# Kernel tuning notes

Hardware: AMD Instinct MI355X
Metric: run time of the kernel (lower is better)

## Reference

```python
import jax, jax.numpy as jnp
import numpy as np

H, D_MODEL, LEN_Q, LEN_K, D_K, D_V = 16, 1024, 2048, 2048, 64, 64
BATCH = 4
SCALE = 1.0 / np.sqrt(float(D_K))


def setup_inputs() -> dict:
    key = jax.random.key(0)
    ks = jax.random.split(key, 10)
    inp = {
        "Q": jax.random.normal(ks[0], (BATCH, LEN_Q, D_MODEL), dtype=jnp.float32),
        "K": jax.random.normal(ks[1], (BATCH, LEN_K, D_MODEL), dtype=jnp.float32),
        "V": jax.random.normal(ks[2], (BATCH, LEN_K, D_MODEL), dtype=jnp.float32),
        "mask": jax.random.randint(ks[3], (BATCH, LEN_K), 0, 2, dtype=jnp.int32),
        # Linear params (torch Linear: y = x @ W.T + b); store W as [in, out].
        "Wq": jax.random.normal(ks[4], (D_MODEL, H * D_K), dtype=jnp.float32) * (1.0 / np.sqrt(D_MODEL)),
        "bq": jnp.zeros((H * D_K,), dtype=jnp.float32),
        "Wk": jax.random.normal(ks[5], (D_MODEL, H * D_K), dtype=jnp.float32) * (1.0 / np.sqrt(D_MODEL)),
        "bk": jnp.zeros((H * D_K,), dtype=jnp.float32),
        "Wv": jax.random.normal(ks[6], (D_MODEL, H * D_V), dtype=jnp.float32) * (1.0 / np.sqrt(D_MODEL)),
        "bv": jnp.zeros((H * D_V,), dtype=jnp.float32),
    }
    return inp


def reference(Q, K, V, mask, Wq, bq, Wk, bk, Wv, bv):
    B = Q.shape[0]
    # Projections -> [B, S, H, d]
    q = (Q @ Wq + bq).reshape(B, LEN_Q, H, D_K)
    k = (K @ Wk + bk).reshape(B, LEN_K, H, D_K)
    v = (V @ Wv + bv).reshape(B, LEN_K, H, D_V)
    # Scores: [B, H, len_q, len_k]
    scores = jnp.einsum("bqhd,bkhd->bhqk", q, k) * SCALE
    # Key-padding mask broadcast over heads and queries
    scores = jnp.where(mask[:, None, None, :] == 0, jnp.float32(-1e9), scores)
    alpha = jax.nn.softmax(scores, axis=-1)
    out = jnp.einsum("bhqk,bkhd->bqhd", alpha, v)  # [B, len_q, H, d_v]
    return out.reshape(B, LEN_Q, H * D_V)
```

## Files before the change

kernel.cpp:

```cpp
#include <hip/hip_runtime.h>

#define NH 16
#define DM 1024
#define SQ 2048
#define BT 4

typedef __attribute__((ext_vector_type(8))) short bf16x8;
typedef __attribute__((ext_vector_type(4))) short sh4;
typedef __attribute__((ext_vector_type(4))) float f4;
typedef __attribute__((ext_vector_type(4))) float fv4;
typedef __attribute__((ext_vector_type(4))) unsigned uv4;
typedef unsigned short u16;

#define M2BIAS 23.083120654f
#define SCALE2 0.18033688f

__device__ __forceinline__ u16 f2bf(float f) {
    union { float f; unsigned u; } v; v.f = f;
    unsigned r = v.u + 0x7FFFu + ((v.u >> 16) & 1u);
    return (u16)(r >> 16);
}

__device__ __forceinline__ float fast_exp2(float x) {
#if __has_builtin(__builtin_amdgcn_exp2f)
    return __builtin_amdgcn_exp2f(x);
#else
    return exp2f(x);
#endif
}

__device__ __forceinline__ int prem(int s) {
    return (s & ~31) | ((s & 4) << 2) | ((s >> 1) & 12) | (s & 3);
}

#define GLD16(gp, lp) __builtin_amdgcn_global_load_lds( \
    (const __attribute__((address_space(1))) void*)(gp), \
    (__attribute__((address_space(3))) void*)(lp), 16, 0, 0)

__global__ __launch_bounds__(256) void cvt_x(const float* __restrict__ x, u16* __restrict__ y) {
    int i = blockIdx.x * 256 + threadIdx.x;
    fv4 v = ((const fv4*)x)[i];
    sh4 r;
    r[0] = (short)f2bf(v[0]); r[1] = (short)f2bf(v[1]);
    r[2] = (short)f2bf(v[2]); r[3] = (short)f2bf(v[3]);
    ((sh4*)y)[i] = r;
}

__global__ __launch_bounds__(256) void cvt_wT(const float* __restrict__ Wsrc, u16* __restrict__ Wt) {
    __shared__ float t[64][65];
    int r0 = blockIdx.x * 64, c0 = blockIdx.y * 64;
    #pragma unroll
    for (int i = 0; i < 16; ++i) {
        int idx = i * 256 + threadIdx.x;
        int r = idx >> 6, c = idx & 63;
        t[r][c] = Wsrc[(size_t)(r0 + r) * DM + c0 + c];
    }
    __syncthreads();
    #pragma unroll
    for (int i = 0; i < 16; ++i) {
        int idx = i * 256 + threadIdx.x;
        int n = idx >> 6, k = idx & 63;
        Wt[(size_t)(c0 + n) * DM + r0 + k] = f2bf(t[k][n]);
    }
}

__global__ __launch_bounds__(256) void mk_mbias(const int* __restrict__ mask, float* __restrict__ mb) {
    int i = blockIdx.x * 256 + threadIdx.x;
    mb[prem(i)] = mask[i] ? -M2BIAS : -__builtin_inff();
}

__global__ __launch_bounds__(256) void gemm_proj(const u16* __restrict__ A, const u16* __restrict__ Bt,
                                                 const float* __restrict__ bias, u16* __restrict__ outp,
                                                 int vmode) {
    __shared__ u16 As[128 * 64];
    __shared__ u16 Bs[128 * 64];
    int tid = threadIdx.x;
    int w = tid >> 6, lane = tid & 63, quad = lane >> 4, l16 = lane & 15;
    int wm = w >> 1, wn = w & 1;
    int r8 = lane >> 3, cg = (lane & 7) ^ r8;
    const u16* Ag = A + (size_t)blockIdx.x * 128 * DM;
    const u16* Bg = Bt + (size_t)blockIdx.y * 128 * DM;

    f4 acc[4][4];
    #pragma unroll
    for (int mt = 0; mt < 4; ++mt)
        #pragma unroll
        for (int nt = 0; nt < 4; ++nt) acc[mt][nt] = f4{0.f, 0.f, 0.f, 0.f};

    for (int kt = 0; kt < 16; ++kt) {
        int kofs = kt * 64 + cg * 8;
        #pragma unroll
        for (int c = 0; c < 4; ++c) {
            int rbase = w * 32 + c * 8;
            GLD16(Ag + (size_t)(rbase + r8) * DM + kofs, &As[rbase * 64]);
            GLD16(Bg + (size_t)(rbase + r8) * DM + kofs, &Bs[rbase * 64]);
        }
        __syncthreads();
        #pragma unroll
        for (int ks = 0; ks < 2; ++ks) {
            bf16x8 afr[4], bfr[4];
            #pragma unroll
            for (int mt = 0; mt < 4; ++mt) {
                int row = wm * 64 + mt * 16 + l16;
                int ch = (ks * 4 + quad) ^ (row & 7);
                afr[mt] = *(const bf16x8*)&As[row * 64 + ch * 8];
            }
            #pragma unroll
            for (int nt = 0; nt < 4; ++nt) {
                int row = wn * 64 + nt * 16 + l16;
                int ch = (ks * 4 + quad) ^ (row & 7);
                bfr[nt] = *(const bf16x8*)&Bs[row * 64 + ch * 8];
            }
            #pragma unroll
            for (int mt = 0; mt < 4; ++mt)
                #pragma unroll
                for (int nt = 0; nt < 4; ++nt)
                    acc[mt][nt] = __builtin_amdgcn_mfma_f32_16x16x32_bf16(afr[mt], bfr[nt], acc[mt][nt], 0, 0, 0);
        }
        __syncthreads();
    }

    #pragma unroll
    for (int nt = 0; nt < 4; ++nt) {
        int ncol = blockIdx.y * 128 + wn * 64 + nt * 16 + l16;
        float bn = bias[ncol];
        int h = ncol >> 6, d = ncol & 63;
        #pragma unroll
        for (int mt = 0; mt < 4; ++mt) {
            int mbase = blockIdx.x * 128 + wm * 64 + mt * 16 + quad * 4;
            int bidx = mbase >> 11, s0 = mbase & 2047;
            if (vmode == 1) {
                sh4 pk;
                #pragma unroll
                for (int reg = 0; reg < 4; ++reg) pk[reg] = (short)f2bf(acc[mt][nt][reg] + bn);
                *(sh4*)&outp[(((size_t)bidx * NH + h) * 64 + d) * SQ + s0] = pk;
            } else {
                int sp = (vmode == 2) ? prem(s0) : s0;
                size_t base = ((size_t)bidx * NH + h) * SQ;
                #pragma unroll
                for (int reg = 0; reg < 4; ++reg)
                    outp[(base + sp + reg) * 64 + d] = f2bf(acc[mt][nt][reg] + bn);
            }
        }
    }
}

__global__ __launch_bounds__(256, 4) void attn(const u16* __restrict__ qw, const u16* __restrict__ kw,
                                               const u16* __restrict__ vtw, const float* __restrict__ mbias,
                                               float* __restrict__ outp) {
    __shared__ u16 Ks[2][64 * 64];
    __shared__ u16 Vs[2][64 * 64];
    int tid = threadIdx.x;
    int w = tid >> 6, lane = tid & 63, quad = lane >> 4, l16 = lane & 15;
    int r8 = lane >> 3, sl = lane & 7;
    int bh = blockIdx.x, b = bh >> 4;
    int h = bh & 15;
    int qbase = blockIdx.y * 128 + w * 32;
    const u16* qp = qw + (size_t)bh * SQ * 64;
    const u16* kp = kw + (size_t)bh * SQ * 64;
    const u16* vp = vtw + (size_t)bh * 64 * SQ;
    const float* mbp = mbias + b * SQ;

    bf16x8 aq[2][2];
    #pragma unroll
    for (int mt = 0; mt < 2; ++mt)
        #pragma unroll
        for (int ks = 0; ks < 2; ++ks)
            aq[mt][ks] = *(const bf16x8*)&qp[(size_t)(qbase + mt * 16 + l16) * 64 + ks * 32 + quad * 8];

    f4 o[2][4];
    float lrow[2] = {0.f, 0.f};
    #pragma unroll
    for (int mt = 0; mt < 2; ++mt)
        #pragma unroll
        for (int nt = 0; nt < 4; ++nt) o[mt][nt] = f4{0.f, 0.f, 0.f, 0.f};

    auto stage = [&](int buf, int k0) {
        #pragma unroll
        for (int j = 0; j < 2; ++j) {
            int row = w * 16 + j * 8 + r8;
            int gsl = sl ^ (row & 7);
            GLD16(kp + (size_t)(k0 + row) * 64 + gsl * 8, &Ks[buf][(w * 16 + j * 8) * 64]);
            GLD16(vp + (size_t)row * SQ + k0 + gsl * 8, &Vs[buf][(w * 16 + j * 8) * 64]);
        }
    };

    stage(0, 0);
    for (int kb = 0; kb < 32; ++kb) {
        int buf = kb & 1;
        int k0 = kb * 64;
        __syncthreads();
        fv4 bias4[4];
        #pragma unroll
        for (int kt = 0; kt < 4; ++kt)
            bias4[kt] = *(const fv4*)&mbp[k0 + kt * 16 + quad * 4];
        if (kb + 1 < 32) stage(buf ^ 1, k0 + 64);

        bf16x8 bk[4][2];
        #pragma unroll
        for (int kt = 0; kt < 4; ++kt)
            #pragma unroll
            for (int ks = 0; ks < 2; ++ks) {
                int r = kt * 16 + l16;
                int slot = (ks * 4 + quad) ^ (r & 7);
                bk[kt][ks] = *(const bf16x8*)&Ks[buf][r * 64 + slot * 8];
            }
        f4 S[4][2];
        #pragma unroll
        for (int kt = 0; kt < 4; ++kt)
            #pragma unroll
            for (int mt = 0; mt < 2; ++mt) {
                f4 s = f4{0.f, 0.f, 0.f, 0.f};
                s = __builtin_amdgcn_mfma_f32_16x16x32_bf16(bk[kt][0], aq[mt][0], s, 0, 0, 0);
                s = __builtin_amdgcn_mfma_f32_16x16x32_bf16(bk[kt][1], aq[mt][1], s, 0, 0, 0);
                S[kt][mt] = s;
            }
        bf16x8 pa8[2][2];
        #pragma unroll
        for (int g = 0; g < 2; ++g)
            #pragma unroll
            for (int mt = 0; mt < 2; ++mt) {
                f4 se = S[2 * g][mt], so = S[2 * g + 1][mt];
                float p0 = fast_exp2(se[0] * SCALE2 + bias4[2 * g][0]);
                float p1 = fast_exp2(se[1] * SCALE2 + bias4[2 * g][1]);
                float p2 = fast_exp2(se[2] * SCALE2 + bias4[2 * g][2]);
                float p3 = fast_exp2(se[3] * SCALE2 + bias4[2 * g][3]);
                float q0 = fast_exp2(so[0] * SCALE2 + bias4[2 * g + 1][0]);
                float q1 = fast_exp2(so[1] * SCALE2 + bias4[2 * g + 1][1]);
                float q2 = fast_exp2(so[2] * SCALE2 + bias4[2 * g + 1][2]);
                float q3 = fast_exp2(so[3] * SCALE2 + bias4[2 * g + 1][3]);
                lrow[mt] += ((p0 + p1) + (p2 + p3)) + ((q0 + q1) + (q2 + q3));
                uv4 wv;
                wv[0] = (__float_as_uint(p1) & 0xFFFF0000u) | (__float_as_uint(p0) >> 16);
                wv[1] = (__float_as_uint(p3) & 0xFFFF0000u) | (__float_as_uint(p2) >> 16);
                wv[2] = (__float_as_uint(q1) & 0xFFFF0000u) | (__float_as_uint(q0) >> 16);
                wv[3] = (__float_as_uint(q3) & 0xFFFF0000u) | (__float_as_uint(q2) >> 16);
                pa8[g][mt] = __builtin_bit_cast(bf16x8, wv);
            }
        #pragma unroll
        for (int g = 0; g < 2; ++g) {
            bf16x8 bv8[4];
            #pragma unroll
            for (int nt = 0; nt < 4; ++nt) {
                int row = nt * 16 + l16;
                int ch = (g * 4 + quad) ^ (row & 7);
                bv8[nt] = *(const bf16x8*)&Vs[buf][row * 64 + ch * 8];
            }
            #pragma unroll
            for (int mt = 0; mt < 2; ++mt)
                #pragma unroll
                for (int nt = 0; nt < 4; ++nt)
                    o[mt][nt] = __builtin_amdgcn_mfma_f32_16x16x32_bf16(pa8[g][mt], bv8[nt], o[mt][nt], 0, 0, 0);
        }
    }

    #pragma unroll
    for (int mt = 0; mt < 2; ++mt) {
        float v = lrow[mt];
        v += __shfl_xor(v, 16);
        v += __shfl_xor(v, 32);
        #pragma unroll
        for (int reg = 0; reg < 4; ++reg) {
            float inv = 1.f / __shfl(v, quad * 4 + reg);
            int row = qbase + mt * 16 + quad * 4 + reg;
            size_t obase = ((size_t)b * SQ + row) * DM + h * 64;
            #pragma unroll
            for (int nt = 0; nt < 4; ++nt)
                outp[obase + nt * 16 + l16] = o[mt][nt][reg] * inv;
        }
    }
}

extern "C" void kernel_launch(void* const* d_in, const int* in_sizes, int n_in,
                              void* d_out, int out_size, void* d_ws, size_t ws_size,
                              hipStream_t stream) {
    (void)in_sizes; (void)n_in; (void)out_size; (void)ws_size;
    const float* Q  = (const float*)d_in[0];
    const float* K  = (const float*)d_in[1];
    const float* V  = (const float*)d_in[2];
    const int* mask = (const int*)d_in[3];
    const float* Wq = (const float*)d_in[4];
    const float* bq = (const float*)d_in[5];
    const float* Wk = (const float*)d_in[6];
    const float* bk = (const float*)d_in[7];
    const float* Wv = (const float*)d_in[8];
    const float* bv = (const float*)d_in[9];
    float* out = (float*)d_out;
    char* ws = (char*)d_ws;
    u16* q_ws = (u16*)(ws);
    u16* k_ws = (u16*)(ws + (size_t)16 * 1024 * 1024);
    u16* v_ws = (u16*)(ws + (size_t)32 * 1024 * 1024);
    u16* xbuf = (u16*)(ws + (size_t)48 * 1024 * 1024);
    u16* wbuf = (u16*)(ws + (size_t)64 * 1024 * 1024);
    float* mb = (float*)(ws + (size_t)48 * 1024 * 1024);

    dim3 gGemm(64, 8), gW(16, 16);
    cvt_x<<<8192, 256, 0, stream>>>(Q, xbuf);
    cvt_wT<<<gW, 256, 0, stream>>>(Wq, wbuf);
    gemm_proj<<<gGemm, 256, 0, stream>>>(xbuf, wbuf, bq, q_ws, 0);
    cvt_x<<<8192, 256, 0, stream>>>(K, xbuf);
    cvt_wT<<<gW, 256, 0, stream>>>(Wk, wbuf);
    gemm_proj<<<gGemm, 256, 0, stream>>>(xbuf, wbuf, bk, k_ws, 2);
    cvt_x<<<8192, 256, 0, stream>>>(V, xbuf);
    cvt_wT<<<gW, 256, 0, stream>>>(Wv, wbuf);
    gemm_proj<<<gGemm, 256, 0, stream>>>(xbuf, wbuf, bv, v_ws, 1);
    mk_mbias<<<32, 256, 0, stream>>>(mask, mb);
    attn<<<dim3(64, 16), 256, 0, stream>>>(q_ws, k_ws, v_ws, mb, out);
}
```

Baseline: 339.1 us.

## Fuse fp32-to-bf16 activation conversion into a batched QKV projection GEMM

Drops the separate cvt_x passes. The projection GEMM now loads fp32 activations into registers, converts them with v_cvt_pk_bf16_f32, and writes them to LDS, prefetching the next k-tile in registers. The three weight transposes and three GEMMs are each batched into a single launch via blockIdx.z. This removes the bf16 intermediate round-trip through memory and cuts launch count, at the cost of more register pressure and a synchronous register-staged A path instead of direct global-to-LDS loads.

```diff
diff --git a/kernel.cpp b/kernel.cpp
--- a/kernel.cpp
+++ b/kernel.cpp
@@ -37,17 +37,11 @@
     (const __attribute__((address_space(1))) void*)(gp), \
     (__attribute__((address_space(3))) void*)(lp), 16, 0, 0)
 
-__global__ __launch_bounds__(256) void cvt_x(const float* __restrict__ x, u16* __restrict__ y) {
-    int i = blockIdx.x * 256 + threadIdx.x;
-    fv4 v = ((const fv4*)x)[i];
-    sh4 r;
-    r[0] = (short)f2bf(v[0]); r[1] = (short)f2bf(v[1]);
-    r[2] = (short)f2bf(v[2]); r[3] = (short)f2bf(v[3]);
-    ((sh4*)y)[i] = r;
-}
-
-__global__ __launch_bounds__(256) void cvt_wT(const float* __restrict__ Wsrc, u16* __restrict__ Wt) {
+__global__ __launch_bounds__(256) void cvt_wT3(const float* __restrict__ W0, const float* __restrict__ W1,
+                                               const float* __restrict__ W2, u16* __restrict__ Wt) {
     __shared__ float t[64][65];
+    const float* Wsrc = blockIdx.z == 0 ? W0 : (blockIdx.z == 1 ? W1 : W2);
+    u16* dst = Wt + (size_t)blockIdx.z * DM * DM;
     int r0 = blockIdx.x * 64, c0 = blockIdx.y * 64;
     #pragma unroll
     for (int i = 0; i < 16; ++i) {
@@ -60,7 +54,7 @@
     for (int i = 0; i < 16; ++i) {
         int idx = i * 256 + threadIdx.x;
         int n = idx >> 6, k = idx & 63;
-        Wt[(size_t)(c0 + n) * DM + r0 + k] = f2bf(t[k][n]);
+        dst[(size_t)(c0 + n) * DM + r0 + k] = f2bf(t[k][n]);
     }
 }
 
@@ -69,31 +63,59 @@
     mb[prem(i)] = mask[i] ? -M2BIAS : -__builtin_inff();
 }
 
-__global__ __launch_bounds__(256) void gemm_proj(const u16* __restrict__ A, const u16* __restrict__ Bt,
-                                                 const float* __restrict__ bias, u16* __restrict__ outp,
-                                                 int vmode) {
+__global__ __launch_bounds__(256, 3) void gemm3(const float* __restrict__ Qf, const float* __restrict__ Kf,
+                                                const float* __restrict__ Vf, const u16* __restrict__ Wt3,
+                                                const float* __restrict__ bq, const float* __restrict__ bk,
+                                                const float* __restrict__ bv, u16* __restrict__ out3) {
     __shared__ u16 As[128 * 64];
     __shared__ u16 Bs[128 * 64];
+    int z = blockIdx.z;
+    const float* Af = z == 0 ? Qf : (z == 1 ? Kf : Vf);
+    const float* bias = z == 0 ? bq : (z == 1 ? bk : bv);
+    int vmode = z == 0 ? 0 : (z == 1 ? 2 : 1);
+    const u16* Bg = Wt3 + (size_t)z * DM * DM + (size_t)blockIdx.y * 128 * DM;
+    u16* outp = out3 + (size_t)z * 8388608u;
+
     int tid = threadIdx.x;
     int w = tid >> 6, lane = tid & 63, quad = lane >> 4, l16 = lane & 15;
     int wm = w >> 1, wn = w & 1;
     int r8 = lane >> 3, cg = (lane & 7) ^ r8;
-    const u16* Ag = A + (size_t)blockIdx.x * 128 * DM;
-    const u16* Bg = Bt + (size_t)blockIdx.y * 128 * DM;
+
+    int arow0 = w * 32 + (lane >> 4);
+    int acol = (lane & 15) * 4;
+    const float* Ag = Af + (size_t)(blockIdx.x * 128 + arow0) * DM + acol;
+    int ach = (lane & 15) >> 1, asub = lane & 1;
 
     f4 acc[4][4];
     #pragma unroll
     for (int mt = 0; mt < 4; ++mt)
         #pragma unroll
         for (int nt = 0; nt < 4; ++nt) acc[mt][nt] = f4{0.f, 0.f, 0.f, 0.f};
+
+    fv4 ar[8];
+    #pragma unroll
+    for (int j = 0; j < 8; ++j) ar[j] = *(const fv4*)(Ag + (size_t)j * 4 * DM);
 
     for (int kt = 0; kt < 16; ++kt) {
         int kofs = kt * 64 + cg * 8;
         #pragma unroll
         for (int c = 0; c < 4; ++c) {
             int rbase = w * 32 + c * 8;
-            GLD16(Ag + (size_t)(rbase + r8) * DM + kofs, &As[rbase * 64]);
             GLD16(Bg + (size_t)(rbase + r8) * DM + kofs, &Bs[rbase * 64]);
+        }
+        #pragma unroll
+        for (int j = 0; j < 8; ++j) {
+            unsigned lo, hi;
+            asm("v_cvt_pk_bf16_f32 %0, %1, %2" : "=v"(lo) : "v"(ar[j][0]), "v"(ar[j][1]));
+            asm("v_cvt_pk_bf16_f32 %0, %1, %2" : "=v"(hi) : "v"(ar[j][2]), "v"(ar[j][3]));
+            int row = arow0 + j * 4;
+            uint2 pk; pk.x = lo; pk.y = hi;
+            *(uint2*)&As[row * 64 + (ach ^ (row & 7)) * 8 + asub * 4] = pk;
+        }
+        if (kt + 1 < 16) {
+            const float* src = Ag + (kt + 1) * 64;
+            #pragma unroll
+            for (int j = 0; j < 8; ++j) ar[j] = *(const fv4*)(src + (size_t)j * 4 * DM);
         }
         __syncthreads();
         #pragma unroll
@@ -287,23 +309,14 @@
     const float* bv = (const float*)d_in[9];
     float* out = (float*)d_out;
     char* ws = (char*)d_ws;
-    u16* q_ws = (u16*)(ws);
-    u16* k_ws = (u16*)(ws + (size_t)16 * 1024 * 1024);
-    u16* v_ws = (u16*)(ws + (size_t)32 * 1024 * 1024);
-    u16* xbuf = (u16*)(ws + (size_t)48 * 1024 * 1024);
-    u16* wbuf = (u16*)(ws + (size_t)64 * 1024 * 1024);
-    float* mb = (float*)(ws + (size_t)48 * 1024 * 1024);
-
-    dim3 gGemm(64, 8), gW(16, 16);
-    cvt_x<<<8192, 256, 0, stream>>>(Q, xbuf);
-    cvt_wT<<<gW, 256, 0, stream>>>(Wq, wbuf);
-    gemm_proj<<<gGemm, 256, 0, stream>>>(xbuf, wbuf, bq, q_ws, 0);
-    cvt_x<<<8192, 256, 0, stream>>>(K, xbuf);
-    cvt_wT<<<gW, 256, 0, stream>>>(Wk, wbuf);
-    gemm_proj<<<gGemm, 256, 0, stream>>>(xbuf, wbuf, bk, k_ws, 2);
-    cvt_x<<<8192, 256, 0, stream>>>(V, xbuf);
-    cvt_wT<<<gW, 256, 0, stream>>>(Wv, wbuf);
-    gemm_proj<<<gGemm, 256, 0, stream>>>(xbuf, wbuf, bv, v_ws, 1);
+    u16* q_ws  = (u16*)(ws);
+    u16* k_ws  = (u16*)(ws + (size_t)16 * 1024 * 1024);
+    u16* v_ws  = (u16*)(ws + (size_t)32 * 1024 * 1024);
+    u16* wbuf3 = (u16*)(ws + (size_t)48 * 1024 * 1024);
+    float* mb  = (float*)(ws + (size_t)54 * 1024 * 1024);
+
+    cvt_wT3<<<dim3(16, 16, 3), 256, 0, stream>>>(Wq, Wk, Wv, wbuf3);
     mk_mbias<<<32, 256, 0, stream>>>(mask, mb);
+    gemm3<<<dim3(64, 8, 3), 256, 0, stream>>>(Q, K, V, wbuf3, bq, bk, bv, q_ws);
     attn<<<dim3(64, 16), 256, 0, stream>>>(q_ws, k_ws, v_ws, mb, out);
 }
```

New measurement: 321.8 us. 5.1% less time.
